# Optimization experiments

Hardware: AMD Instinct MI355X
Metric: run time of the kernel (lower is better)

The kernel has to match this reference:

```python
import jax, jax.numpy as jnp
import numpy as np
from jax import lax

NUM_CLASSES = 1000
IN_FEATURES = 64 * 8 * 8  # 4096


def _conv2d(x, w, b):
    # x: [B,C,H,W], w: [O,C,3,3], padding=1 (SAME for 3x3 stride 1)
    y = lax.conv_general_dilated(
        x, w, window_strides=(1, 1), padding=((1, 1), (1, 1)),
        dimension_numbers=("NCHW", "OIHW", "NCHW"))
    return y + b[None, :, None, None]


def _maxpool2(x):
    # 2x2 maxpool, stride 2, NCHW
    return lax.reduce_window(x, -jnp.inf, lax.max,
                             (1, 1, 2, 2), (1, 1, 2, 2), "VALID")


def setup_inputs() -> dict:
    key = jax.random.key(0)
    ks = jax.random.split(key, 6)
    B = 4096
    x = jax.random.normal(ks[0], (B, 3, 32, 32), dtype=jnp.float32)
    # PyTorch-default-like param scales (kaiming-ish fan-in bounds approximated by scaled normals)
    w1 = jax.random.normal(ks[1], (32, 3, 3, 3), dtype=jnp.float32) * (1.0 / np.sqrt(3 * 9))
    b1 = jax.random.normal(ks[2], (32,), dtype=jnp.float32) * 0.01
    w2 = jax.random.normal(ks[3], (64, 32, 3, 3), dtype=jnp.float32) * (1.0 / np.sqrt(32 * 9))
    b2 = jax.random.normal(ks[4], (64,), dtype=jnp.float32) * 0.01
    centroids = jax.random.normal(ks[5], (NUM_CLASSES, IN_FEATURES), dtype=jnp.float32)
    return {"x": x, "w1": w1, "b1": b1, "w2": w2, "b2": b2, "centroids": centroids}


def reference(x, w1, b1, w2, b2, centroids):
    # Conv stack: conv3x3 -> relu -> maxpool2 -> conv3x3 -> relu -> maxpool2
    h = _maxpool2(jax.nn.relu(_conv2d(x, w1, b1)))          # [B,32,16,16]
    h = _maxpool2(jax.nn.relu(_conv2d(h, w2, b2)))          # [B,64,8,8]
    f = h.reshape(h.shape[0], -1)                            # [B,4096] (C*H*W order, matches torch .view)
    # Voronoi: L2 distance to centroids, argmin. Same math as
    # ||f[:,None,:] - c[None,:,:]||_2 but computed via the GEMM identity
    # ||f-c||^2 = ||f||^2 - 2 f.c + ||c||^2 (avoids the [B,K,D] tensor).
    f2 = jnp.sum(f * f, axis=1, keepdims=True)               # [B,1]
    c2 = jnp.sum(centroids * centroids, axis=1)[None, :]     # [1,K]
    d2 = f2 - 2.0 * jnp.einsum("bd,kd->bk", f, centroids) + c2
    dist = jnp.sqrt(jnp.maximum(d2, 0.0))                    # [B,K]
    return jnp.argmin(dist, axis=1)                          # [B] int
```

## Files before the change

### kernel.cpp

```cpp
#include <hip/hip_runtime.h>
#include <hip/hip_bf16.h>
#include <stdint.h>

#define THREADS 256

typedef unsigned short u16;
typedef __attribute__((ext_vector_type(8))) short bf16x8;
typedef __attribute__((ext_vector_type(4))) float f32x4;

__device__ inline u16 f2bf(float x) {
    __bf16 b = (__bf16)x;
    return __builtin_bit_cast(u16, b);
}
__device__ inline float bf2f(u16 h) { return __uint_as_float(((unsigned)h) << 16); }

__device__ inline float dpp_xor1(float v) {
    int r = __builtin_amdgcn_mov_dpp(__float_as_int(v), 0xB1, 0xF, 0xF, true);
    return __int_as_float(r);
}

__device__ inline void load_lds16(const void* g, void* l) {
    __builtin_amdgcn_global_load_lds(
        (const __attribute__((address_space(1))) unsigned int*)g,
        (__attribute__((address_space(3))) unsigned int*)l, 16, 0, 0);
}

__global__ __launch_bounds__(256) void prep_w_kernel(
    const float* __restrict__ w1, const float* __restrict__ w2,
    u16* __restrict__ w1t, u16* __restrict__ w2t)
{
    if (blockIdx.x < 8) {
        int idx = blockIdx.x * 256 + threadIdx.x;
        int j     = idx & 7;
        int lane  = (idx >> 3) & 63;
        int mt    = (idx >> 9) & 1;
        int plane = (idx >> 10) & 1;
        int oc = mt * 16 + (lane & 15);
        int k = (lane >> 4) * 8 + j;
        float v = 0.0f;
        if (k < 27) { int ic = k / 9, tap = k - ic * 9; v = w1[oc * 27 + ic * 9 + tap]; }
        u16 hb = f2bf(v);
        w1t[idx] = plane ? f2bf(v - bf2f(hb)) : hb;
    } else {
        int idx = (blockIdx.x - 8) * 256 + threadIdx.x;
        int j     = idx & 7;
        int lane  = (idx >> 3) & 63;
        int mt    = (idx >> 9) & 3;
        int plane = (idx >> 11) & 1;
        int tap   = idx >> 12;
        int oc = mt * 16 + (lane & 15);
        int ic = (lane >> 4) * 8 + j;
        float v = w2[(size_t)oc * 288 + ic * 9 + tap];
        u16 hb = f2bf(v);
        w2t[idx] = plane ? f2bf(v - bf2f(hb)) : hb;
    }
}

#define XSN (3 * 34 * 34)

__global__ __launch_bounds__(256, 3) void conv_fused_kernel(
    const float* __restrict__ x,
    const u16* __restrict__ w1t, const float* __restrict__ b1,
    const u16* __restrict__ w2t, const float* __restrict__ b2,
    u16* __restrict__ f_hi, u16* __restrict__ f_lo,
    const float* __restrict__ cent, u16* __restrict__ c_hi,
    u16* __restrict__ c_lo, float* __restrict__ c2)
{
    const int tid = threadIdx.x;
    const int b = blockIdx.x;

    if (b >= 4096) {
        __shared__ float wsum[4];
        const int n = b - 4096;
        const size_t base = (size_t)n * 4096;
        float s = 0.0f;
        #pragma unroll
        for (int q = 0; q < 4; ++q) {
            int e = (tid + q * 256) * 4;
            float4 v = *(const float4*)(cent + base + e);
            s = fmaf(v.x, v.x, s); s = fmaf(v.y, v.y, s);
            s = fmaf(v.z, v.z, s); s = fmaf(v.w, v.w, s);
            ushort4 h, l;
            h.x = f2bf(v.x); l.x = f2bf(v.x - bf2f(h.x));
            h.y = f2bf(v.y); l.y = f2bf(v.y - bf2f(h.y));
            h.z = f2bf(v.z); l.z = f2bf(v.z - bf2f(h.z));
            h.w = f2bf(v.w); l.w = f2bf(v.w - bf2f(h.w));
            *(ushort4*)(c_hi + base + e) = h;
            *(ushort4*)(c_lo + base + e) = l;
        }
        #pragma unroll
        for (int off = 32; off >= 1; off >>= 1) s += __shfl_down(s, off, 64);
        int lane = tid & 63, wv = tid >> 6;
        if (lane == 0) wsum[wv] = s;
        __syncthreads();
        if (tid == 0) c2[n] = wsum[0] + wsum[1] + wsum[2] + wsum[3];
        return;
    }

    __shared__ __align__(16) unsigned xsi[XSN];
    __shared__ __align__(16) u16 h1hi[16 * 16 * 32];
    __shared__ __align__(16) u16 h1lo[16 * 16 * 32];

    const int lane = tid & 63;
    const int li = lane & 15, ls = lane >> 4;
    const int wv = tid >> 6;
    __builtin_assume(li >= 0 && li < 16);
    __builtin_assume(ls >= 0 && ls < 4);
    __builtin_assume(wv >= 0 && wv < 4);

    for (int i = tid; i < XSN; i += THREADS) xsi[i] = 0u;
    __syncthreads();

    const float* xb = x + (size_t)b * 3072;
    #pragma unroll
    for (int q = 0; q < 3; ++q) {
        int idx = tid + q * THREADS;
        int ic  = idx >> 8;
        int rem = idx & 255;
        int y   = rem >> 3;
        int x4  = (rem & 7) << 2;
        float4 v = *(const float4*)(xb + ic * 1024 + y * 32 + x4);
        int base = ic * 1156 + (1 + y) * 34 + 1 + x4;
        float vv[4] = {v.x, v.y, v.z, v.w};
        #pragma unroll
        for (int e = 0; e < 4; ++e) {
            u16 hb = f2bf(vv[e]);
            u16 lb = f2bf(vv[e] - bf2f(hb));
            xsi[base + e] = (unsigned)hb | ((unsigned)lb << 16);
        }
    }
    __syncthreads();

    {
        bf16x8 aH1[2], aL1[2];
        #pragma unroll
        for (int mt = 0; mt < 2; ++mt) {
            aH1[mt] = *(const bf16x8*)(w1t + (size_t)((0 * 2 + mt) * 64 + lane) * 8);
            aL1[mt] = *(const bf16x8*)(w1t + (size_t)((1 * 2 + mt) * 64 + lane) * 8);
        }
        int koffc[8];
        #pragma unroll
        for (int j = 0; j < 8; ++j) {
            int k = ls * 8 + j;
            int kc = (k < 27) ? k : 0;
            int ic = kc / 9, tap = kc - ic * 9;
            int ky = tap / 3, kx = tap - ky * 3;
            koffc[j] = ic * 1156 + ky * 34 + kx;
        }
        float b1v[2][4];
        #pragma unroll
        for (int mt = 0; mt < 2; ++mt)
            #pragma unroll
            for (int reg = 0; reg < 4; ++reg)
                b1v[mt][reg] = b1[16 * mt + 4 * ls + reg];

        #pragma unroll
        for (int q = 0; q < 4; ++q) {
            f32x4 acc[4][2];
            #pragma unroll
            for (int s = 0; s < 4; ++s)
                #pragma unroll
                for (int mt = 0; mt < 2; ++mt)
                    acc[s][mt] = (f32x4){b1v[mt][0], b1v[mt][1], b1v[mt][2], b1v[mt][3]};

            #pragma unroll
            for (int s = 0; s < 4; ++s) {
                int y = 8 * wv + 2 * q + (s >> 1);
                int xcol = 16 * (s & 1) + li;
                int base = y * 34 + xcol;
                bf16x8 bH, bL;
                #pragma unroll
                for (int j = 0; j < 8; ++j) {
                    unsigned dw = xsi[base + koffc[j]];
                    bH[j] = (short)(u16)(dw & 0xffffu);
                    bL[j] = (short)(u16)(dw >> 16);
                }
                #pragma unroll
                for (int mt = 0; mt < 2; ++mt) {
                    acc[s][mt] = __builtin_amdgcn_mfma_f32_16x16x32_bf16(aH1[mt], bH, acc[s][mt], 0, 0, 0);
                    acc[s][mt] = __builtin_amdgcn_mfma_f32_16x16x32_bf16(aH1[mt], bL, acc[s][mt], 0, 0, 0);
                    acc[s][mt] = __builtin_amdgcn_mfma_f32_16x16x32_bf16(aL1[mt], bH, acc[s][mt], 0, 0, 0);
                }
            }
            int py = 4 * wv + q;
            #pragma unroll
            for (int h = 0; h < 2; ++h) {
                #pragma unroll
                for (int mt = 0; mt < 2; ++mt) {
                    ushort4 pH, pL;
                    #pragma unroll
                    for (int reg = 0; reg < 4; ++reg) {
                        float v0 = acc[h][mt][reg];
                        float v1 = acc[h + 2][mt][reg];
                        float m0 = fmaxf(v0, dpp_xor1(v0));
                        float m1 = fmaxf(v1, dpp_xor1(v1));
                        float v = fmaxf(fmaxf(m0, m1), 0.0f);
                        u16 hb = f2bf(v);
                        ((u16*)&pH)[reg] = hb;
                        ((u16*)&pL)[reg] = f2bf(v - bf2f(hb));
                    }
                    if ((li & 1) == 0) {
                        int px = (li >> 1) + 8 * h;
                        int ib = 2 * mt + (ls >> 1);
                        int byte = (py * 16 + px) * 64 + ((ib ^ ((px >> 1) & 3)) << 4) + (ls & 1) * 8;
                        *(ushort4*)((char*)h1hi + byte) = pH;
                        *(ushort4*)((char*)h1lo + byte) = pL;
                    }
                }
            }
        }
    }
    __syncthreads();

    {
        const bf16x8 zf = {0, 0, 0, 0, 0, 0, 0, 0};

        float b2v[4][4];
        #pragma unroll
        for (int mt = 0; mt < 4; ++mt)
            #pragma unroll
            for (int reg = 0; reg < 4; ++reg)
                b2v[mt][reg] = b2[mt * 16 + ls * 4 + reg];

        f32x4 acc[4][4];
        #pragma unroll
        for (int mt = 0; mt < 4; ++mt)
            #pragma unroll
            for (int ntl = 0; ntl < 4; ++ntl)
                acc[mt][ntl] = (f32x4){b2v[mt][0], b2v[mt][1], b2v[mt][2], b2v[mt][3]};

        #pragma unroll
        for (int kx = 0; kx < 3; ++kx) {
            int xg = li + kx - 1;
            bool xo = (unsigned)xg > 15u;
            int xc = min(max(xg, 0), 15);
            int slotb = (ls ^ ((xc >> 1) & 3)) << 4;

            bf16x8 cH[5], cL[5];
            #pragma unroll
            for (int d = 0; d < 5; ++d) {
                int yg = 4 * wv + d;
                if (yg <= 15) {
                    int byte = (yg * 16 + xc) * 64 + slotb;
                    bf16x8 h = *(const bf16x8*)((const char*)h1hi + byte);
                    bf16x8 l = *(const bf16x8*)((const char*)h1lo + byte);
                    cH[d] = xo ? zf : h;
                    cL[d] = xo ? zf : l;
                } else { cH[d] = zf; cL[d] = zf; }
            }

            #pragma unroll
            for (int ky = 0; ky < 3; ++ky) {
                const int tap = ky * 3 + kx;
                bf16x8 aH[4], aL[4];
                #pragma unroll
                for (int mt = 0; mt < 4; ++mt) {
                    aH[mt] = *(const bf16x8*)(w2t + (size_t)(tap * 4096 + mt * 512 + lane * 8));
                    aL[mt] = *(const bf16x8*)(w2t + (size_t)(tap * 4096 + 2048 + mt * 512 + lane * 8));
                }
                #pragma unroll
                for (int ntl = 0; ntl < 4; ++ntl) {
                    int d = ntl + ky - 1;
                    int yg = 4 * wv + d;
                    if ((unsigned)yg > 15u) continue;
                    bf16x8 bH, bL;
                    if (d == -1 || d == 5) {
                        int byte = (yg * 16 + xc) * 64 + slotb;
                        bH = *(const bf16x8*)((const char*)h1hi + byte);
                        bL = *(const bf16x8*)((const char*)h1lo + byte);
                        if (xo) { bH = zf; bL = zf; }
                    } else {
                        bH = cH[d]; bL = cL[d];
                    }
                    #pragma unroll
                    for (int mt = 0; mt < 4; ++mt) {
                        acc[mt][ntl] = __builtin_amdgcn_mfma_f32_16x16x32_bf16(aH[mt], bH, acc[mt][ntl], 0, 0, 0);
                        acc[mt][ntl] = __builtin_amdgcn_mfma_f32_16x16x32_bf16(aH[mt], bL, acc[mt][ntl], 0, 0, 0);
                        acc[mt][ntl] = __builtin_amdgcn_mfma_f32_16x16x32_bf16(aL[mt], bH, acc[mt][ntl], 0, 0, 0);
                    }
                }
            }
        }

        const size_t fbase = (size_t)b * 4096;
        #pragma unroll
        for (int mt = 0; mt < 4; ++mt) {
            #pragma unroll
            for (int reg = 0; reg < 4; ++reg) {
                int oc = mt * 16 + ls * 4 + reg;
                #pragma unroll
                for (int p = 0; p < 2; ++p) {
                    float v0 = acc[mt][2 * p + 0][reg];
                    float v1 = acc[mt][2 * p + 1][reg];
                    float x0 = fmaxf(v0, dpp_xor1(v0));
                    float x1 = fmaxf(v1, dpp_xor1(v1));
                    float v = fmaxf(fmaxf(x0, x1), 0.0f);
                    if ((li & 1) == 0) {
                        int py = 2 * wv + p, px = li >> 1;
                        u16 hb = f2bf(v);
                        u16 lb = f2bf(v - bf2f(hb));
                        size_t o = fbase + (size_t)oc * 64 + py * 8 + px;
                        f_hi[o] = hb;
                        f_lo[o] = lb;
                    }
                }
            }
        }
    }
}

#define GBM 128
#define GBN 64
#define GBK 32

__global__ __launch_bounds__(256, 2) void gemm_argmin_mfma(
    const u16* __restrict__ f_hi, const u16* __restrict__ f_lo,
    const u16* __restrict__ c_hi, const u16* __restrict__ c_lo,
    const float* __restrict__ c2, unsigned long long* __restrict__ packed)
{
    __shared__ __align__(16) u16 Ah[GBM * GBK];
    __shared__ __align__(16) u16 Al[GBM * GBK];
    __shared__ __align__(16) u16 Bh[GBN * GBK];
    __shared__ __align__(16) u16 Bl[GBN * GBK];
    __shared__ unsigned long long red[GBM];

    const int tid = threadIdx.x;
    const int id = blockIdx.x;
    const int xcd = id & 7;
    const int g = id >> 3;
    const int mb = xcd * 4 + (g & 3);
    const int nb = g >> 2;
    const int m0 = mb * GBM;
    const int n0 = nb * GBN;

    const int lane = tid & 63;
    const int wid  = tid >> 6;
    const int wm = wid >> 1, wn = wid & 1;
    const int li = lane & 15;
    const int ls = lane >> 4;
    const int swz = (li >> 1) & 3;
    const int rslot = (ls ^ swz) << 4;

    if (tid < GBM) red[tid] = ~0ULL;

    f32x4 acc[4][2];
    #pragma unroll
    for (int i = 0; i < 4; ++i)
        #pragma unroll
        for (int j = 0; j < 2; ++j) acc[i][j] = (f32x4){0.f, 0.f, 0.f, 0.f};

    for (int k0 = 0; k0 < 4096; k0 += GBK) {
        #pragma unroll
        for (int q = 0; q < 2; ++q) {
            int idx = tid + q * 256;
            int row = idx >> 2, slot = idx & 3;
            int kg = k0 + ((slot ^ ((row >> 1) & 3)) << 3);
            size_t goff = (size_t)(m0 + row) * 4096 + kg;
            load_lds16(f_hi + goff, &Ah[idx * 8]);
            load_lds16(f_lo + goff, &Al[idx * 8]);
        }
        {
            int idx = tid;
            int row = idx >> 2, slot = idx & 3;
            int kg = k0 + ((slot ^ ((row >> 1) & 3)) << 3);
            size_t goff = (size_t)(n0 + row) * 4096 + kg;
            load_lds16(c_hi + goff, &Bh[idx * 8]);
            load_lds16(c_lo + goff, &Bl[idx * 8]);
        }
        __syncthreads();

        bf16x8 ah[4], al[4], bh[2], bl[2];
        #pragma unroll
        for (int mt = 0; mt < 4; ++mt) {
            int r = wm * 64 + mt * 16 + li;
            int byte = r * 64 + rslot;
            ah[mt] = *(const bf16x8*)((const char*)Ah + byte);
            al[mt] = *(const bf16x8*)((const char*)Al + byte);
        }
        #pragma unroll
        for (int nt = 0; nt < 2; ++nt) {
            int r = wn * 32 + nt * 16 + li;
            int byte = r * 64 + rslot;
            bh[nt] = *(const bf16x8*)((const char*)Bh + byte);
            bl[nt] = *(const bf16x8*)((const char*)Bl + byte);
        }
        #pragma unroll
        for (int mt = 0; mt < 4; ++mt)
            #pragma unroll
            for (int nt = 0; nt < 2; ++nt) {
                acc[mt][nt] = __builtin_amdgcn_mfma_f32_16x16x32_bf16(ah[mt], bh[nt], acc[mt][nt], 0, 0, 0);
                acc[mt][nt] = __builtin_amdgcn_mfma_f32_16x16x32_bf16(ah[mt], bl[nt], acc[mt][nt], 0, 0, 0);
                acc[mt][nt] = __builtin_amdgcn_mfma_f32_16x16x32_bf16(al[mt], bh[nt], acc[mt][nt], 0, 0, 0);
            }
        __syncthreads();
    }

    #pragma unroll
    for (int mt = 0; mt < 4; ++mt) {
        #pragma unroll
        for (int reg = 0; reg < 4; ++reg) {
            unsigned long long best = ~0ULL;
            #pragma unroll
            for (int nt = 0; nt < 2; ++nt) {
                int n = n0 + wn * 32 + nt * 16 + li;
                if (n < 1000) {
                    float v = c2[n] - 2.0f * acc[mt][nt][reg];
                    unsigned bi = __float_as_uint(v);
                    bi = (bi & 0x80000000u) ? ~bi : (bi | 0x80000000u);
                    unsigned long long key = ((unsigned long long)bi << 32) | (unsigned)n;
                    if (key < best) best = key;
                }
            }
            #pragma unroll
            for (int d = 1; d < 16; d <<= 1) {
                unsigned long long o = __shfl_xor(best, d, 64);
                if (o < best) best = o;
            }
            if (li == 0) {
                int lr = wm * 64 + mt * 16 + ls * 4 + reg;
                atomicMin(&red[lr], best);
            }
        }
    }
    __syncthreads();
    if (tid < GBM) atomicMin(&packed[m0 + tid], red[tid]);
}

__global__ __launch_bounds__(256) void extract_kernel(
    const unsigned long long* __restrict__ packed, int* __restrict__ out)
{
    int i = blockIdx.x * 256 + threadIdx.x;
    out[i] = (int)(unsigned)(packed[i] & 0xFFFFFFFFull);
}

extern "C" void kernel_launch(void* const* d_in, const int* in_sizes, int n_in,
                              void* d_out, int out_size, void* d_ws, size_t ws_size,
                              hipStream_t stream)
{
    const float* x    = (const float*)d_in[0];
    const float* w1   = (const float*)d_in[1];
    const float* b1   = (const float*)d_in[2];
    const float* w2   = (const float*)d_in[3];
    const float* b2   = (const float*)d_in[4];
    const float* cent = (const float*)d_in[5];
    int* out = (int*)d_out;

    char* ws = (char*)d_ws;
    u16* f_hi = (u16*)(ws);
    u16* f_lo = (u16*)(ws + 33554432);
    u16* c_hi = (u16*)(ws + 67108864);
    u16* c_lo = (u16*)(ws + 75497472);
    float* c2 = (float*)(ws + 83886080);
    unsigned long long* packed =
        (unsigned long long*)(ws + 83890176);
    u16* w1t = (u16*)(ws + 83922944);
    u16* w2t = (u16*)(ws + 83927040);

    hipMemsetAsync(packed, 0xFF, 4096 * sizeof(unsigned long long), stream);
    prep_w_kernel<<<152, 256, 0, stream>>>(w1, w2, w1t, w2t);
    conv_fused_kernel<<<5096, 256, 0, stream>>>(x, w1t, b1, w2t, b2, f_hi, f_lo,
                                                cent, c_hi, c_lo, c2);
    gemm_argmin_mfma<<<512, 256, 0, stream>>>(f_hi, f_lo, c_hi, c_lo, c2, packed);
    extract_kernel<<<16, 256, 0, stream>>>(packed, out);
}
```

Measured before the change: 251.3 us.

## Double-buffer LDS tiles in GEMM-argmin kernel to overlap loads with MFMA

Splits the K-loop into separate stage and compute steps over two LDS buffers. The global-to-LDS loads for the next K tile are issued before the MFMAs on the current tile, and only one barrier per iteration remains instead of two, so memory latency can hide behind compute. LDS use doubles to about 48KB per block, which may limit occupancy at 2 blocks per CU. Correctness relies on the direct-to-LDS loads being complete by the end-of-iteration barrier.

```diff
diff --git a/kernel.cpp b/kernel.cpp
--- a/kernel.cpp
+++ b/kernel.cpp
@@ -318,10 +318,10 @@
     const u16* __restrict__ c_hi, const u16* __restrict__ c_lo,
     const float* __restrict__ c2, unsigned long long* __restrict__ packed)
 {
-    __shared__ __align__(16) u16 Ah[GBM * GBK];
-    __shared__ __align__(16) u16 Al[GBM * GBK];
-    __shared__ __align__(16) u16 Bh[GBN * GBK];
-    __shared__ __align__(16) u16 Bl[GBN * GBK];
+    __shared__ __align__(16) u16 Ah[2][GBM * GBK];
+    __shared__ __align__(16) u16 Al[2][GBM * GBK];
+    __shared__ __align__(16) u16 Bh[2][GBN * GBK];
+    __shared__ __align__(16) u16 Bl[2][GBN * GBK];
     __shared__ unsigned long long red[GBM];
 
     const int tid = threadIdx.x;
@@ -341,48 +341,47 @@
     const int swz = (li >> 1) & 3;
     const int rslot = (ls ^ swz) << 4;
 
-    if (tid < GBM) red[tid] = ~0ULL;
-
     f32x4 acc[4][2];
     #pragma unroll
     for (int i = 0; i < 4; ++i)
         #pragma unroll
         for (int j = 0; j < 2; ++j) acc[i][j] = (f32x4){0.f, 0.f, 0.f, 0.f};
 
-    for (int k0 = 0; k0 < 4096; k0 += GBK) {
+    auto STAGE = [&](int buf, int k0) {
         #pragma unroll
         for (int q = 0; q < 2; ++q) {
             int idx = tid + q * 256;
             int row = idx >> 2, slot = idx & 3;
             int kg = k0 + ((slot ^ ((row >> 1) & 3)) << 3);
             size_t goff = (size_t)(m0 + row) * 4096 + kg;
-            load_lds16(f_hi + goff, &Ah[idx * 8]);
-            load_lds16(f_lo + goff, &Al[idx * 8]);
+            load_lds16(f_hi + goff, &Ah[buf][idx * 8]);
+            load_lds16(f_lo + goff, &Al[buf][idx * 8]);
         }
         {
             int idx = tid;
             int row = idx >> 2, slot = idx & 3;
             int kg = k0 + ((slot ^ ((row >> 1) & 3)) << 3);
             size_t goff = (size_t)(n0 + row) * 4096 + kg;
-            load_lds16(c_hi + goff, &Bh[idx * 8]);
-            load_lds16(c_lo + goff, &Bl[idx * 8]);
-        }
-        __syncthreads();
-
+            load_lds16(c_hi + goff, &Bh[buf][idx * 8]);
+            load_lds16(c_lo + goff, &Bl[buf][idx * 8]);
+        }
+    };
+
+    auto COMPUTE = [&](int buf) {
         bf16x8 ah[4], al[4], bh[2], bl[2];
         #pragma unroll
         for (int mt = 0; mt < 4; ++mt) {
             int r = wm * 64 + mt * 16 + li;
             int byte = r * 64 + rslot;
-            ah[mt] = *(const bf16x8*)((const char*)Ah + byte);
-            al[mt] = *(const bf16x8*)((const char*)Al + byte);
+            ah[mt] = *(const bf16x8*)((const char*)&Ah[buf][0] + byte);
+            al[mt] = *(const bf16x8*)((const char*)&Al[buf][0] + byte);
         }
         #pragma unroll
         for (int nt = 0; nt < 2; ++nt) {
             int r = wn * 32 + nt * 16 + li;
             int byte = r * 64 + rslot;
-            bh[nt] = *(const bf16x8*)((const char*)Bh + byte);
-            bl[nt] = *(const bf16x8*)((const char*)Bl + byte);
+            bh[nt] = *(const bf16x8*)((const char*)&Bh[buf][0] + byte);
+            bl[nt] = *(const bf16x8*)((const char*)&Bl[buf][0] + byte);
         }
         #pragma unroll
         for (int mt = 0; mt < 4; ++mt)
@@ -392,8 +391,20 @@
                 acc[mt][nt] = __builtin_amdgcn_mfma_f32_16x16x32_bf16(ah[mt], bl[nt], acc[mt][nt], 0, 0, 0);
                 acc[mt][nt] = __builtin_amdgcn_mfma_f32_16x16x32_bf16(al[mt], bh[nt], acc[mt][nt], 0, 0, 0);
             }
+    };
+
+    STAGE(0, 0);
+    if (tid < GBM) red[tid] = ~0ULL;
+    __syncthreads();
+
+    int cur = 0;
+    for (int t = 0; t < 127; ++t) {
+        STAGE(cur ^ 1, (t + 1) * GBK);
+        COMPUTE(cur);
         __syncthreads();
-    }
+        cur ^= 1;
+    }
+    COMPUTE(cur);
 
     #pragma unroll
     for (int mt = 0; mt < 4; ++mt) {
```

Result: slower. 284.4 us (+13.1%).
